# Kernel optimization log

Measured on AMD Instinct MI355X. Metric: run time of the kernel, lower is better.

The kernel has to match this reference:

```python
import jax, jax.numpy as jnp
import numpy as np

IN_DIM = 2
HID = 256
OUT_DIM = 1
B = 131072


def setup_inputs() -> dict:
    key = jax.random.key(0)
    ks = jax.random.split(key, 9)
    def glorot(k, shape):
        fan_in = shape[0]
        return jax.random.normal(k, shape, dtype=jnp.float32) / jnp.sqrt(jnp.float32(fan_in))
    return {
        "x": jax.random.normal(ks[0], (B, IN_DIM), dtype=jnp.float32),
        "W1": glorot(ks[1], (IN_DIM, HID)), "b1": jnp.zeros((HID,), jnp.float32),
        "W2": glorot(ks[2], (HID, HID)),    "b2": jnp.zeros((HID,), jnp.float32),
        "W3": glorot(ks[3], (HID, HID)),    "b3": jnp.zeros((HID,), jnp.float32),
        "W4": glorot(ks[4], (HID, OUT_DIM)),"b4": jnp.zeros((OUT_DIM,), jnp.float32),
    }


def reference(x, W1, b1, W2, b2, W3, b3, W4, b4):
    # Inner PINN model: tanh MLP, per-sample fn (IN_DIM,) -> (OUT_DIM,)
    def f(xi):
        h = jnp.tanh(xi @ W1 + b1)
        h = jnp.tanh(h @ W2 + b2)
        h = jnp.tanh(h @ W3 + b3)
        return h @ W4 + b4

    # Original layer computes full batch_jacobian then slices column 0.
    # Mathematically this is the directional derivative along e0, computed
    # here directly with forward-mode JVPs (same values, no wasted columns).
    e0 = jnp.zeros((IN_DIM,), x.dtype).at[0].set(1.0)

    def du_dx0(xi):  # (OUT_DIM,) : d u / d x[0]
        return jax.jvp(f, (xi,), (e0,))[1]

    def per_point(xi):
        u = f(xi)                                   # (OUT_DIM,)
        du, d2u = jax.jvp(du_dx0, (xi,), (e0,))     # du/dx0, d2u/dx0^2
        return u, du, d2u

    return jax.vmap(per_point)(x)  # each (B, OUT_DIM)
```

## Files before the change

### kernel.cpp

```cpp
#include <hip/hip_runtime.h>


#define HID 256
#define TM  32

typedef _Float16 half8 __attribute__((ext_vector_type(8)));
typedef _Float16 half4 __attribute__((ext_vector_type(4)));
typedef float    f32x4 __attribute__((ext_vector_type(4)));

#define MFMA16 __builtin_amdgcn_mfma_f32_16x16x32_f16

__device__ __forceinline__ float fast_tanh(float z) {
    const float e = __expf(2.0f * z);
#if __has_builtin(__builtin_amdgcn_rcpf)
    const float r = __builtin_amdgcn_rcpf(e + 1.0f);
#else
    const float r = 1.0f / (e + 1.0f);
#endif
    return fmaf(-2.0f, r, 1.0f);
}

__global__ __launch_bounds__(256) void prep_w(const float* __restrict__ W2,
                                              const float* __restrict__ W3,
                                              _Float16* __restrict__ wsf) {
    const int t = blockIdx.x * 256 + threadIdx.x;
    const float* __restrict__ W = (t >> 13) ? W3 : W2;
    _Float16* dst = wsf + (size_t)(t >> 13) * 65536;
    const int r     = t & 8191;
    const int kc    = r >> 10;
    const int strip = (r >> 6) & 15;
    const int lane  = r & 63;
    const int row   = kc * 32 + ((lane >> 4) << 3);
    const int col   = strip * 16 + (lane & 15);
    half8 vh;
    #pragma unroll
    for (int j = 0; j < 8; ++j)
        vh[j] = (_Float16)W[(size_t)(row + j) * HID + col];
    *(half8*)&dst[(size_t)r * 8] = vh;
}

__global__ __launch_bounds__(256, 2) void pinn_mfma(
    const float* __restrict__ x,
    const float* __restrict__ W1, const float* __restrict__ b1,
    const float* __restrict__ b2, const float* __restrict__ b3,
    const float* __restrict__ W4, const float* __restrict__ b4,
    const _Float16* __restrict__ wsf,
    float* __restrict__ out, int B)
{
    __shared__ __align__(16) _Float16 Ahi[3 * 32 * 256];
    __shared__ float psumW[4][3][TM];

    const int tid  = threadIdx.x;
    const int s0   = blockIdx.x * TM;
    const int lane = tid & 63;
    const int wave = tid >> 6;

    {
        const int m  = (tid & 7) | (((tid >> 3) & 3) << 3);
        const int k0 = (tid >> 5) << 5;
        const float2 xv = *(const float2*)&x[(size_t)(s0 + m) * 2];
        const float x0 = xv.x, x1 = xv.y;
        half8 vh[3][4];
        #pragma unroll
        for (int q = 0; q < 4; ++q) {
            #pragma unroll
            for (int h = 0; h < 2; ++h) {
                const int n = k0 + q * 8 + h * 4;
                const f32x4 w0 = *(const f32x4*)&W1[n];
                const f32x4 w1 = *(const f32x4*)&W1[HID + n];
                const f32x4 bb = *(const f32x4*)&b1[n];
                #pragma unroll
                for (int r = 0; r < 4; ++r) {
                    const float z  = fmaf(x0, w0[r], fmaf(x1, w1[r], bb[r]));
                    const float a  = fast_tanh(z);
                    const float sN = 1.0f - a * a;
                    const float ad  = sN * w0[r];
                    const float add = -2.0f * a * ad * w0[r];
                    vh[0][q][h * 4 + r] = (_Float16)a;
                    vh[1][q][h * 4 + r] = (_Float16)ad;
                    vh[2][q][h * 4 + r] = (_Float16)add;
                }
            }
        }
        const int rkm = m & 7;
        const int g0  = k0 >> 3;
        #pragma unroll
        for (int s = 0; s < 3; ++s)
            #pragma unroll
            for (int q = 0; q < 4; ++q)
                *(half8*)&Ahi[s * 8192 + m * 256 + (((g0 + q) ^ rkm) << 3)] = vh[s][q];
    }
    __syncthreads();

    const int ml = lane & 15;
    const int hi = lane >> 4;
    const int rk = ml & 7;
    const int u4 = hi << 2;
    const _Float16* __restrict__ Arow = &Ahi[ml * 256];

    #pragma unroll 1
    for (int layer = 0; layer < 2; ++layer) {
        const _Float16* __restrict__ Wl =
            wsf + ((size_t)layer << 16) + (wave << 11) + (lane << 3);

        f32x4 acc[3][4][2];
        #pragma unroll
        for (int s = 0; s < 3; ++s)
            #pragma unroll
            for (int nt = 0; nt < 4; ++nt)
                #pragma unroll
                for (int mt = 0; mt < 2; ++mt)
                    acc[s][nt][mt] = (f32x4){0.f, 0.f, 0.f, 0.f};

        half8 wcur[4];
        #pragma unroll
        for (int nt = 0; nt < 4; ++nt)
            wcur[nt] = *(const half8*)&Wl[nt << 9];

        #pragma unroll 1
        for (int kc = 0; kc < 8; ++kc) {
            const int kn = (kc < 7) ? kc + 1 : 7;
            const _Float16* __restrict__ Wk = Wl + (kn << 13);
            half8 wnxt[4];
            #pragma unroll
            for (int nt = 0; nt < 4; ++nt)
                wnxt[nt] = *(const half8*)&Wk[nt << 9];

            const _Float16* __restrict__ Ap =
                Arow + ((((kc << 2) | hi) ^ rk) << 3);
            half8 af[3][2];
            #pragma unroll
            for (int s = 0; s < 3; ++s)
                #pragma unroll
                for (int mt = 0; mt < 2; ++mt)
                    af[s][mt] = *(const half8*)&Ap[s * 8192 + mt * 4096];

            #pragma unroll
            for (int nt = 0; nt < 4; ++nt)
                #pragma unroll
                for (int mt = 0; mt < 2; ++mt) {
                    acc[0][nt][mt] = MFMA16(wcur[nt], af[0][mt], acc[0][nt][mt], 0, 0, 0);
                    acc[1][nt][mt] = MFMA16(wcur[nt], af[1][mt], acc[1][nt][mt], 0, 0, 0);
                    acc[2][nt][mt] = MFMA16(wcur[nt], af[2][mt], acc[2][nt][mt], 0, 0, 0);
                }
            #pragma unroll
            for (int nt = 0; nt < 4; ++nt) wcur[nt] = wnxt[nt];
        }

        if (layer == 0) {
            __syncthreads();
            #pragma unroll
            for (int nt = 0; nt < 4; ++nt) {
                const int ub  = (wave << 6) + (nt << 4) + u4;
                const f32x4 bb = *(const f32x4*)&b2[ub];
                const int gsw = (((ub >> 3) ^ rk) << 3) + (u4 & 4);
                #pragma unroll
                for (int mt = 0; mt < 2; ++mt) {
                    half4 hv[3];
                    #pragma unroll
                    for (int r = 0; r < 4; ++r) {
                        const float z   = acc[0][nt][mt][r] + bb[r];
                        const float a   = fast_tanh(z);
                        const float sN  = 1.0f - a * a;
                        const float zd  = acc[1][nt][mt][r];
                        const float zdd = acc[2][nt][mt][r];
                        const float ad  = sN * zd;
                        const float add = fmaf(sN, zdd, -2.0f * a * ad * zd);
                        hv[0][r] = (_Float16)a;
                        hv[1][r] = (_Float16)ad;
                        hv[2][r] = (_Float16)add;
                    }
                    const int base = (mt * 16 + ml) * 256 + gsw;
                    *(half4*)&Ahi[base]         = hv[0];
                    *(half4*)&Ahi[8192  + base] = hv[1];
                    *(half4*)&Ahi[16384 + base] = hv[2];
                }
            }
            __syncthreads();
        } else {
            float pd[3][2] = {{0.f, 0.f}, {0.f, 0.f}, {0.f, 0.f}};
            #pragma unroll
            for (int nt = 0; nt < 4; ++nt) {
                const int ub = (wave << 6) + (nt << 4) + u4;
                const f32x4 bb = *(const f32x4*)&b3[ub];
                const f32x4 w4 = *(const f32x4*)&W4[ub];
                #pragma unroll
                for (int mt = 0; mt < 2; ++mt) {
                    #pragma unroll
                    for (int r = 0; r < 4; ++r) {
                        const float z   = acc[0][nt][mt][r] + bb[r];
                        const float a   = fast_tanh(z);
                        const float sN  = 1.0f - a * a;
                        const float zd  = acc[1][nt][mt][r];
                        const float zdd = acc[2][nt][mt][r];
                        const float ad  = sN * zd;
                        const float add = fmaf(sN, zdd, -2.0f * a * ad * zd);
                        pd[0][mt] = fmaf(a,   w4[r], pd[0][mt]);
                        pd[1][mt] = fmaf(ad,  w4[r], pd[1][mt]);
                        pd[2][mt] = fmaf(add, w4[r], pd[2][mt]);
                    }
                }
            }
            #pragma unroll
            for (int s = 0; s < 3; ++s)
                #pragma unroll
                for (int mt = 0; mt < 2; ++mt) {
                    pd[s][mt] += __shfl_xor(pd[s][mt], 16, 64);
                    pd[s][mt] += __shfl_xor(pd[s][mt], 32, 64);
                }
            if (lane < 16) {
                #pragma unroll
                for (int s = 0; s < 3; ++s) {
                    psumW[wave][s][lane]      = pd[s][0];
                    psumW[wave][s][16 + lane] = pd[s][1];
                }
            }
        }
    }
    __syncthreads();

    if (tid < 96) {
        const int s = tid >> 5;
        const int m = tid & 31;
        const float v = psumW[0][s][m] + psumW[1][s][m]
                      + psumW[2][s][m] + psumW[3][s][m]
                      + ((s == 0) ? b4[0] : 0.0f);
        out[(size_t)s * B + s0 + m] = v;
    }
}

extern "C" void kernel_launch(void* const* d_in, const int* in_sizes, int n_in,
                              void* d_out, int out_size, void* d_ws, size_t ws_size,
                              hipStream_t stream) {
    const float* x  = (const float*)d_in[0];
    const float* W1 = (const float*)d_in[1];
    const float* b1 = (const float*)d_in[2];
    const float* W2 = (const float*)d_in[3];
    const float* b2 = (const float*)d_in[4];
    const float* W3 = (const float*)d_in[5];
    const float* b3 = (const float*)d_in[6];
    const float* W4 = (const float*)d_in[7];
    const float* b4 = (const float*)d_in[8];
    float* out = (float*)d_out;

    const int B = in_sizes[0] / 2;

    prep_w<<<64, 256, 0, stream>>>(W2, W3, (_Float16*)d_ws);
    pinn_mfma<<<B / TM, 256, 0, stream>>>(x, W1, b1, b2, b3, W4, b4,
                                          (const _Float16*)d_ws, out, B);
}
```

Measured before the change: 174.8 us.

## Halve per-block sample tile to 16 rows and raise occupancy to 4 blocks/CU

Reduces samples per block from 32 to 16, halving the LDS activation buffer and MFMA accumulators, and raises the launch-bounds occupancy hint from 2 to 4 blocks per CU. The k-loop drops its software-prefetched weight double buffer in favour of full unrolling with direct loads, and wraps the MFMA group in s_setprio. Each weight fragment loaded from global/L2 is now reused across half as many samples, doubling weight traffic per sample, in exchange for more waves to hide latency. The grid doubles in size; the launch code is not shown and presumably derives its block count from TM.

```diff
diff --git a/kernel.cpp b/kernel.cpp
--- a/kernel.cpp
+++ b/kernel.cpp
@@ -2,7 +2,7 @@
 
 
 #define HID 256
-#define TM  32
+#define TM  16
 
 typedef _Float16 half8 __attribute__((ext_vector_type(8)));
 typedef _Float16 half4 __attribute__((ext_vector_type(4)));
@@ -39,7 +39,7 @@
     *(half8*)&dst[(size_t)r * 8] = vh;
 }
 
-__global__ __launch_bounds__(256, 2) void pinn_mfma(
+__global__ __launch_bounds__(256, 4) void pinn_mfma(
     const float* __restrict__ x,
     const float* __restrict__ W1, const float* __restrict__ b1,
     const float* __restrict__ b2, const float* __restrict__ b3,
@@ -47,7 +47,7 @@
     const _Float16* __restrict__ wsf,
     float* __restrict__ out, int B)
 {
-    __shared__ __align__(16) _Float16 Ahi[3 * 32 * 256];
+    __shared__ __align__(16) _Float16 Ahi[3 * 16 * 256];
     __shared__ float psumW[4][3][TM];
 
     const int tid  = threadIdx.x;
@@ -56,13 +56,13 @@
     const int wave = tid >> 6;
 
     {
-        const int m  = (tid & 7) | (((tid >> 3) & 3) << 3);
-        const int k0 = (tid >> 5) << 5;
+        const int m  = tid & 15;
+        const int k0 = (tid >> 4) << 4;
         const float2 xv = *(const float2*)&x[(size_t)(s0 + m) * 2];
         const float x0 = xv.x, x1 = xv.y;
-        half8 vh[3][4];
-        #pragma unroll
-        for (int q = 0; q < 4; ++q) {
+        half8 vh[3][2];
+        #pragma unroll
+        for (int q = 0; q < 2; ++q) {
             #pragma unroll
             for (int h = 0; h < 2; ++h) {
                 const int n = k0 + q * 8 + h * 4;
@@ -83,12 +83,12 @@
             }
         }
         const int rkm = m & 7;
-        const int g0  = k0 >> 3;
+        const int g0w = k0 >> 3;
         #pragma unroll
         for (int s = 0; s < 3; ++s)
             #pragma unroll
-            for (int q = 0; q < 4; ++q)
-                *(half8*)&Ahi[s * 8192 + m * 256 + (((g0 + q) ^ rkm) << 3)] = vh[s][q];
+            for (int q = 0; q < 2; ++q)
+                *(half8*)&Ahi[s * 4096 + m * 256 + (((g0w + q) ^ rkm) << 3)] = vh[s][q];
     }
     __syncthreads();
 
@@ -103,48 +103,34 @@
         const _Float16* __restrict__ Wl =
             wsf + ((size_t)layer << 16) + (wave << 11) + (lane << 3);
 
-        f32x4 acc[3][4][2];
+        f32x4 acc[3][4];
         #pragma unroll
         for (int s = 0; s < 3; ++s)
             #pragma unroll
             for (int nt = 0; nt < 4; ++nt)
-                #pragma unroll
-                for (int mt = 0; mt < 2; ++mt)
-                    acc[s][nt][mt] = (f32x4){0.f, 0.f, 0.f, 0.f};
-
-        half8 wcur[4];
-        #pragma unroll
-        for (int nt = 0; nt < 4; ++nt)
-            wcur[nt] = *(const half8*)&Wl[nt << 9];
-
-        #pragma unroll 1
+                acc[s][nt] = (f32x4){0.f, 0.f, 0.f, 0.f};
+
+        #pragma unroll
         for (int kc = 0; kc < 8; ++kc) {
-            const int kn = (kc < 7) ? kc + 1 : 7;
-            const _Float16* __restrict__ Wk = Wl + (kn << 13);
-            half8 wnxt[4];
-            #pragma unroll
-            for (int nt = 0; nt < 4; ++nt)
-                wnxt[nt] = *(const half8*)&Wk[nt << 9];
-
             const _Float16* __restrict__ Ap =
                 Arow + ((((kc << 2) | hi) ^ rk) << 3);
-            half8 af[3][2];
-            #pragma unroll
-            for (int s = 0; s < 3; ++s)
-                #pragma unroll
-                for (int mt = 0; mt < 2; ++mt)
-                    af[s][mt] = *(const half8*)&Ap[s * 8192 + mt * 4096];
-
+            const half8 af0 = *(const half8*)&Ap[0];
+            const half8 af1 = *(const half8*)&Ap[4096];
+            const half8 af2 = *(const half8*)&Ap[8192];
+            const _Float16* __restrict__ Wk = Wl + (kc << 13);
+            half8 wf[4];
             #pragma unroll
             for (int nt = 0; nt < 4; ++nt)
-                #pragma unroll
-                for (int mt = 0; mt < 2; ++mt) {
-                    acc[0][nt][mt] = MFMA16(wcur[nt], af[0][mt], acc[0][nt][mt], 0, 0, 0);
-                    acc[1][nt][mt] = MFMA16(wcur[nt], af[1][mt], acc[1][nt][mt], 0, 0, 0);
-                    acc[2][nt][mt] = MFMA16(wcur[nt], af[2][mt], acc[2][nt][mt], 0, 0, 0);
-                }
-            #pragma unroll
-            for (int nt = 0; nt < 4; ++nt) wcur[nt] = wnxt[nt];
+                wf[nt] = *(const half8*)&Wk[nt << 9];
+
+            __builtin_amdgcn_s_setprio(1);
+            #pragma unroll
+            for (int nt = 0; nt < 4; ++nt) {
+                acc[0][nt] = MFMA16(wf[nt], af0, acc[0][nt], 0, 0, 0);
+                acc[1][nt] = MFMA16(wf[nt], af1, acc[1][nt], 0, 0, 0);
+                acc[2][nt] = MFMA16(wf[nt], af2, acc[2][nt], 0, 0, 0);
+            }
+            __builtin_amdgcn_s_setprio(0);
         }
 
         if (layer == 0) {
@@ -154,74 +140,64 @@
                 const int ub  = (wave << 6) + (nt << 4) + u4;
                 const f32x4 bb = *(const f32x4*)&b2[ub];
                 const int gsw = (((ub >> 3) ^ rk) << 3) + (u4 & 4);
-                #pragma unroll
-                for (int mt = 0; mt < 2; ++mt) {
-                    half4 hv[3];
-                    #pragma unroll
-                    for (int r = 0; r < 4; ++r) {
-                        const float z   = acc[0][nt][mt][r] + bb[r];
-                        const float a   = fast_tanh(z);
-                        const float sN  = 1.0f - a * a;
-                        const float zd  = acc[1][nt][mt][r];
-                        const float zdd = acc[2][nt][mt][r];
-                        const float ad  = sN * zd;
-                        const float add = fmaf(sN, zdd, -2.0f * a * ad * zd);
-                        hv[0][r] = (_Float16)a;
-                        hv[1][r] = (_Float16)ad;
-                        hv[2][r] = (_Float16)add;
-                    }
-                    const int base = (mt * 16 + ml) * 256 + gsw;
-                    *(half4*)&Ahi[base]         = hv[0];
-                    *(half4*)&Ahi[8192  + base] = hv[1];
-                    *(half4*)&Ahi[16384 + base] = hv[2];
+                half4 hv[3];
+                #pragma unroll
+                for (int r = 0; r < 4; ++r) {
+                    const float z   = acc[0][nt][r] + bb[r];
+                    const float a   = fast_tanh(z);
+                    const float sN  = 1.0f - a * a;
+                    const float zd  = acc[1][nt][r];
+                    const float zdd = acc[2][nt][r];
+                    const float ad  = sN * zd;
+                    const float add = fmaf(sN, zdd, -2.0f * a * ad * zd);
+                    hv[0][r] = (_Float16)a;
+                    hv[1][r] = (_Float16)ad;
+                    hv[2][r] = (_Float16)add;
                 }
+                const int base = ml * 256 + gsw;
+                *(half4*)&Ahi[base]        = hv[0];
+                *(half4*)&Ahi[4096 + base] = hv[1];
+                *(half4*)&Ahi[8192 + base] = hv[2];
             }
             __syncthreads();
         } else {
-            float pd[3][2] = {{0.f, 0.f}, {0.f, 0.f}, {0.f, 0.f}};
+            float pd[3] = {0.f, 0.f, 0.f};
             #pragma unroll
             for (int nt = 0; nt < 4; ++nt) {
                 const int ub = (wave << 6) + (nt << 4) + u4;
                 const f32x4 bb = *(const f32x4*)&b3[ub];
                 const f32x4 w4 = *(const f32x4*)&W4[ub];
                 #pragma unroll
-                for (int mt = 0; mt < 2; ++mt) {
-                    #pragma unroll
-                    for (int r = 0; r < 4; ++r) {
-                        const float z   = acc[0][nt][mt][r] + bb[r];
-                        const float a   = fast_tanh(z);
-                        const float sN  = 1.0f - a * a;
-                        const float zd  = acc[1][nt][mt][r];
-                        const float zdd = acc[2][nt][mt][r];
-                        const float ad  = sN * zd;
-                        const float add = fmaf(sN, zdd, -2.0f * a * ad * zd);
-                        pd[0][mt] = fmaf(a,   w4[r], pd[0][mt]);
-                        pd[1][mt] = fmaf(ad,  w4[r], pd[1][mt]);
-                        pd[2][mt] = fmaf(add, w4[r], pd[2][mt]);
-                    }
+                for (int r = 0; r < 4; ++r) {
+                    const float z   = acc[0][nt][r] + bb[r];
+                    const float a   = fast_tanh(z);
+                    const float sN  = 1.0f - a * a;
+                    const float zd  = acc[1][nt][r];
+                    const float zdd = acc[2][nt][r];
+                    const float ad  = sN * zd;
+                    const float add = fmaf(sN, zdd, -2.0f * a * ad * zd);
+                    pd[0] = fmaf(a,   w4[r], pd[0]);
+                    pd[1] = fmaf(ad,  w4[r], pd[1]);
+                    pd[2] = fmaf(add, w4[r], pd[2]);
                 }
             }
             #pragma unroll
-            for (int s = 0; s < 3; ++s)
-                #pragma unroll
-                for (int mt = 0; mt < 2; ++mt) {
-                    pd[s][mt] += __shfl_xor(pd[s][mt], 16, 64);
-                    pd[s][mt] += __shfl_xor(pd[s][mt], 32, 64);
-                }
+            for (int s = 0; s < 3; ++s) {
+                pd[s] += __shfl_xor(pd[s], 16, 64);
+                pd[s] += __shfl_xor(pd[s], 32, 64);
+            }
             if (lane < 16) {
                 #pragma unroll
-                for (int s = 0; s < 3; ++s) {
-                    psumW[wave][s][lane]      = pd[s][0];
-                    psumW[wave][s][16 + lane] = pd[s][1];
-                }
+                for (int s = 0; s < 3; ++s)
+                    psumW[wave][s][lane] = pd[s];
             }
         }
     }
     __syncthreads();
 
-    if (tid < 96) {
-        const int s = tid >> 5;
-        const int m = tid & 31;
+    if (tid < 48) {
+        const int s = tid >> 4;
+        const int m = tid & 15;
         const float v = psumW[0][s][m] + psumW[1][s][m]
                       + psumW[2][s][m] + psumW[3][s][m]
                       + ((s == 0) ? b4[0] : 0.0f);
```

After: 191.9 us. 9.8% more time.

## Drop register double-buffering of weights, add MFMA priority, vectorize weight prep

Applied to the files above, without the earlier changes.

The weight prep kernel now reads each row of W2/W3 with coalesced float4 loads and scatters the halves into the MFMA fragment layout, using twice as many threads. In the main kernel, the cross-iteration weight prefetch (wcur/wnxt) is replaced by loading the current k-chunk's weights just before the MFMAs, which lowers register pressure. The MFMA burst is wrapped in s_setprio to favour the matrix issue. A barrier is added after every layer. The risk is that weight load latency is no longer hidden, and the dead wnxt loads may or may not be removed by the compiler.

```diff
diff --git a/kernel.cpp b/kernel.cpp
--- a/kernel.cpp
+++ b/kernel.cpp
@@ -24,19 +24,23 @@
                                               const float* __restrict__ W3,
                                               _Float16* __restrict__ wsf) {
     const int t = blockIdx.x * 256 + threadIdx.x;
-    const float* __restrict__ W = (t >> 13) ? W3 : W2;
-    _Float16* dst = wsf + (size_t)(t >> 13) * 65536;
-    const int r     = t & 8191;
-    const int kc    = r >> 10;
-    const int strip = (r >> 6) & 15;
-    const int lane  = r & 63;
-    const int row   = kc * 32 + ((lane >> 4) << 3);
-    const int col   = strip * 16 + (lane & 15);
-    half8 vh;
+    const float* __restrict__ W = (t >> 14) ? W3 : W2;
+    _Float16* __restrict__ dst = wsf + (size_t)(t >> 14) * 65536;
+    const int r    = t & 16383;
+    const int row  = r >> 6;
+    const int col0 = (r & 63) << 2;
+    const f32x4 v = *(const f32x4*)&W[(size_t)row * HID + col0];
+    const int kc = row >> 5;
+    const int hi = (row >> 3) & 3;
+    const int j  = row & 7;
     #pragma unroll
-    for (int j = 0; j < 8; ++j)
-        vh[j] = (_Float16)W[(size_t)(row + j) * HID + col];
-    *(half8*)&dst[(size_t)r * 8] = vh;
+    for (int c = 0; c < 4; ++c) {
+        const int col   = col0 + c;
+        const int strip = col >> 4;
+        const int ml    = col & 15;
+        dst[((size_t)((kc * 16 + strip) * 64 + hi * 16 + ml) << 3) + j] =
+            (_Float16)v[c];
+    }
 }
 
 __global__ __launch_bounds__(256, 2) void pinn_mfma(
@@ -112,11 +116,6 @@
                 for (int mt = 0; mt < 2; ++mt)
                     acc[s][nt][mt] = (f32x4){0.f, 0.f, 0.f, 0.f};
 
-        half8 wcur[4];
-        #pragma unroll
-        for (int nt = 0; nt < 4; ++nt)
-            wcur[nt] = *(const half8*)&Wl[nt << 9];
-
         #pragma unroll 1
         for (int kc = 0; kc < 8; ++kc) {
             const int kn = (kc < 7) ? kc + 1 : 7;
@@ -135,20 +134,28 @@
                 for (int mt = 0; mt < 2; ++mt)
                     af[s][mt] = *(const half8*)&Ap[s * 8192 + mt * 4096];
 
-            #pragma unroll
-            for (int nt = 0; nt < 4; ++nt)
-                #pragma unroll
-                for (int mt = 0; mt < 2; ++mt) {
-                    acc[0][nt][mt] = MFMA16(wcur[nt], af[0][mt], acc[0][nt][mt], 0, 0, 0);
-                    acc[1][nt][mt] = MFMA16(wcur[nt], af[1][mt], acc[1][nt][mt], 0, 0, 0);
-                    acc[2][nt][mt] = MFMA16(wcur[nt], af[2][mt], acc[2][nt][mt], 0, 0, 0);
-                }
-            #pragma unroll
-            for (int nt = 0; nt < 4; ++nt) wcur[nt] = wnxt[nt];
+            const _Float16* __restrict__ Wc = Wl + (kc << 13);
+            half8 wf[4];
+            #pragma unroll
+            for (int nt = 0; nt < 4; ++nt)
+                wf[nt] = *(const half8*)&Wc[nt << 9];
+
+            __builtin_amdgcn_s_setprio(1);
+            #pragma unroll
+            for (int nt = 0; nt < 4; ++nt)
+                #pragma unroll
+                for (int mt = 0; mt < 2; ++mt) {
+                    acc[0][nt][mt] = MFMA16(wf[nt], af[0][mt], acc[0][nt][mt], 0, 0, 0);
+                    acc[1][nt][mt] = MFMA16(wf[nt], af[1][mt], acc[1][nt][mt], 0, 0, 0);
+                    acc[2][nt][mt] = MFMA16(wf[nt], af[2][mt], acc[2][nt][mt], 0, 0, 0);
+                }
+            __builtin_amdgcn_s_setprio(0);
+            (void)wnxt;
         }
 
+        __syncthreads();
+
         if (layer == 0) {
-            __syncthreads();
             #pragma unroll
             for (int nt = 0; nt < 4; ++nt) {
                 const int ub  = (wave << 6) + (nt << 4) + u4;
@@ -245,7 +252,7 @@
 
     const int B = in_sizes[0] / 2;
 
-    prep_w<<<64, 256, 0, stream>>>(W2, W3, (_Float16*)d_ws);
+    prep_w<<<128, 256, 0, stream>>>(W2, W3, (_Float16*)d_ws);
     pinn_mfma<<<B / TM, 256, 0, stream>>>(x, W1, b1, b2, b3, W4, b4,
                                           (const _Float16*)d_ws, out, B);
 }
```

After: 180.3 us. 3.2% more time.
